# Kernel optimization log

Hardware: AMD Instinct MI355X
Metric: run time of the kernel (lower is better)

## Reference

```python
import jax, jax.numpy as jnp
import numpy as np
import math

B, T, C = 32, 256, 1024
LAYER_ID, NUM_LAYERS = 12, 24
NEG_INF = -1e38


def setup_inputs() -> dict:
    key = jax.random.key(0)
    ks = jax.random.split(key, 5)
    x = jax.random.normal(ks[0], (B, T, C), dtype=jnp.float32)
    # deterministic parameter init, faithful to the torch __init__
    r01 = LAYER_ID / (NUM_LAYERS - 1)          # ratio_0_to_1
    r10 = 1.0 - LAYER_ID / NUM_LAYERS          # ratio_1_to_almost0
    h = jnp.arange(C, dtype=jnp.float32)
    time_decay = -5.0 + 8.0 * (h / (C - 1)) ** (0.7 + 1.3 * r01)
    tf = (jnp.arange(C) + 1) % 3 - 1
    time_first = jnp.full((C,), math.log(0.3), jnp.float32) + 0.5 * tf.astype(jnp.float32)
    xr = (jnp.arange(C, dtype=jnp.float32) / C)[None, None, :]   # [1,1,C]
    time_mix_k = xr ** r10
    time_mix_v = xr ** r10 + 0.3 * r01
    time_mix_r = xr ** (0.5 * r10)
    s = 1.0 / math.sqrt(C)
    Wk = jax.random.normal(ks[1], (C, C), jnp.float32) * s
    Wv = jax.random.normal(ks[2], (C, C), jnp.float32) * s
    Wr = jax.random.normal(ks[3], (C, C), jnp.float32) * s
    Wo = jax.random.normal(ks[4], (C, C), jnp.float32) * s
    return {"x": x, "time_decay": time_decay, "time_first": time_first,
            "time_mix_k": time_mix_k, "time_mix_v": time_mix_v, "time_mix_r": time_mix_r,
            "Wk": Wk, "Wv": Wv, "Wr": Wr, "Wo": Wo}


def wkv(time_decay, time_first, k, v):
    """Numerically-stabilized WKV scan. k,v: [B,T,C]; decay/first: [C]."""
    w = -jnp.exp(time_decay)   # per-channel log-decay (negative)
    u = time_first
    kT = jnp.swapaxes(k, 0, 1)  # [T,B,C]
    vT = jnp.swapaxes(v, 0, 1)

    def step(carry, kv):
        p, q, o = carry                       # p,q: running num/den; o: log scale
        kt, vt = kv                           # [B,C]
        no = jnp.maximum(o, u + kt)
        A = jnp.exp(o - no)
        Bc = jnp.exp(u + kt - no)
        y = (A * p + Bc * vt) / (A * q + Bc)
        no2 = jnp.maximum(w + o, kt)
        A2 = jnp.exp(w + o - no2)
        B2 = jnp.exp(kt - no2)
        return (A2 * p + B2 * vt, A2 * q + B2, no2), y

    init = (jnp.zeros((k.shape[0], k.shape[2]), k.dtype),
            jnp.zeros((k.shape[0], k.shape[2]), k.dtype),
            jnp.full((k.shape[0], k.shape[2]), NEG_INF, k.dtype))
    _, yT = jax.lax.scan(step, init, (kT, vT))
    return jnp.swapaxes(yT, 0, 1)  # [B,T,C]


def reference(x, time_decay, time_first, time_mix_k, time_mix_v, time_mix_r, Wk, Wv, Wr, Wo):
    # time_shift: xx[t] = x[t-1], xx[0] = 0
    xx = jnp.pad(x, ((0, 0), (1, 0), (0, 0)))[:, :-1, :]
    xk = x * time_mix_k + xx * (1.0 - time_mix_k)
    xv = x * time_mix_v + xx * (1.0 - time_mix_v)
    xr = x * time_mix_r + xx * (1.0 - time_mix_r)
    k = jnp.einsum('btc,dc->btd', xk, Wk)
    v = jnp.einsum('btc,dc->btd', xv, Wv)
    r = jnp.einsum('btc,dc->btd', xr, Wr)
    sr = jax.nn.sigmoid(r)
    rwkv = sr * wkv(time_decay, time_first, k, v)
    return jnp.einsum('btc,dc->btd', rwkv, Wo)
```

## Files before the change

kernel.cpp:

```cpp
#include <hip/hip_runtime.h>

#define Bdim 32
#define Tdim 256
#define Cdim 1024

typedef unsigned short u16;
typedef unsigned int u32;
typedef __bf16 bf16x8 __attribute__((ext_vector_type(8)));
typedef float f32x4 __attribute__((ext_vector_type(4)));

__device__ __forceinline__ float bf2f(u32 u) {
    union { u32 i; float f; } v; v.i = u << 16; return v.f;
}
__device__ __forceinline__ u16 f2bf(float f) {
    union { float f; u32 i; } v; v.f = f;
    u32 u = v.i;
    return (u16)((u + 0x7fffu + ((u >> 16) & 1u)) >> 16);
}

__device__ __forceinline__ void gload16(const u16* g, u16* l) {
    __builtin_amdgcn_global_load_lds(
        (__attribute__((address_space(1))) const void*)g,
        (__attribute__((address_space(3))) void*)l, 16, 0, 0);
}

__global__ __launch_bounds__(256) void prep_fused(
    const float* __restrict__ x, const float* __restrict__ tmk,
    const float* __restrict__ tmv, const float* __restrict__ tmr,
    u16* __restrict__ xk, u16* __restrict__ xv, u16* __restrict__ xr,
    const float* __restrict__ w0, const float* __restrict__ w1,
    const float* __restrict__ w2, const float* __restrict__ w3,
    u16* __restrict__ o0, u16* __restrict__ o1,
    u16* __restrict__ o2, u16* __restrict__ o3)
{
    int bid = blockIdx.x;
    if (bid < 4096) {
        int tid = bid * 256 + threadIdx.x;
        int e = tid << 3;
        int c = e & (Cdim - 1);
        int t = (e >> 10) & (Tdim - 1);
        float xf[8], xxf[8], mk[8], mv[8], mr[8];
        *(float4*)(xf)     = *(const float4*)(x + e);
        *(float4*)(xf + 4) = *(const float4*)(x + e + 4);
        if (t != 0) {
            *(float4*)(xxf)     = *(const float4*)(x + e - Cdim);
            *(float4*)(xxf + 4) = *(const float4*)(x + e - Cdim + 4);
        } else {
#pragma unroll
            for (int j = 0; j < 8; j++) xxf[j] = 0.f;
        }
        *(float4*)(mk)     = *(const float4*)(tmk + c);
        *(float4*)(mk + 4) = *(const float4*)(tmk + c + 4);
        *(float4*)(mv)     = *(const float4*)(tmv + c);
        *(float4*)(mv + 4) = *(const float4*)(tmv + c + 4);
        *(float4*)(mr)     = *(const float4*)(tmr + c);
        *(float4*)(mr + 4) = *(const float4*)(tmr + c + 4);
        u16 ok[8], ov[8], orr[8];
#pragma unroll
        for (int j = 0; j < 8; j++) {
            float d = xf[j] - xxf[j];
            ok[j]  = f2bf(xxf[j] + d * mk[j]);
            ov[j]  = f2bf(xxf[j] + d * mv[j]);
            orr[j] = f2bf(xxf[j] + d * mr[j]);
        }
        *(uint4*)(xk + e) = *(const uint4*)ok;
        *(uint4*)(xv + e) = *(const uint4*)ov;
        *(uint4*)(xr + e) = *(const uint4*)orr;
    } else {
        int wb = bid - 4096;
        int m = wb >> 9;
        const float* src; u16* dst;
        switch (m) {
            case 0: src = w0; dst = o0; break;
            case 1: src = w1; dst = o1; break;
            case 2: src = w2; dst = o2; break;
            default: src = w3; dst = o3; break;
        }
        int i = (((wb & 511) << 8) + threadIdx.x) << 3;
        float a[8];
        *(float4*)(a)     = *(const float4*)(src + i);
        *(float4*)(a + 4) = *(const float4*)(src + i + 4);
        u16 o[8];
#pragma unroll
        for (int j = 0; j < 8; j++) o[j] = f2bf(a[j]);
        *(uint4*)(dst + i) = *(const uint4*)o;
    }
}

template <int BF16OUT>
__device__ __forceinline__ void gemm_body(
    const u16* __restrict__ A, const u16* __restrict__ Bw, void* __restrict__ Cout,
    u16* __restrict__ Ls, int bm, int bn)
{
    const int K = Cdim, N = Cdim;
    const int NT = K / 64;
    const int tid = threadIdx.x;
    const int lane = tid & 63, wave = tid >> 6;
    const int wm = (wave & 1) << 6, wn = (wave >> 1) << 6;
    const int fr = lane & 15, quad = lane >> 4;

    const int srow = tid >> 2;
    const int skc = ((((tid & 3) + ((tid >> 3) & 3)) & 3) << 3);
    const u16* ga = A + (size_t)(bm * 128 + srow) * K + skc;
    const u16* gb = Bw + (size_t)(bn * 128 + srow) * K + skc;
    const size_t gstep = (size_t)64 * K;
    const int lw = wave << 9;

    auto stage = [&](int t, int buf) {
        const u16* gat = ga + t * 64;
        const u16* gbt = gb + t * 64;
        u16* base = Ls + buf * 16384 + lw;
        gload16(gat,              base);
        gload16(gat + gstep,      base + 2048);
        gload16(gbt,              base + 4096);
        gload16(gbt + gstep,      base + 4096 + 2048);
        gload16(gat + 32,         base + 8192);
        gload16(gat + 32 + gstep, base + 8192 + 2048);
        gload16(gbt + 32,         base + 12288);
        gload16(gbt + 32 + gstep, base + 12288 + 2048);
    };

    f32x4 acc[4][4];
#pragma unroll
    for (int i = 0; i < 4; i++)
#pragma unroll
        for (int j = 0; j < 4; j++)
            acc[i][j] = (f32x4){0.f, 0.f, 0.f, 0.f};

    const int rq = (((quad - ((fr >> 1) & 3)) & 3) << 3);

    stage(0, 0);
    asm volatile("s_waitcnt vmcnt(0)" ::: "memory");
    __builtin_amdgcn_s_barrier();

#pragma unroll 1
    for (int t = 0; t < NT; ++t) {
        const int buf = t & 1;
        if (t + 1 < NT) stage(t + 1, buf ^ 1);
        const u16* __restrict__ Tb = Ls + buf * 16384;
#pragma unroll
        for (int h = 0; h < 2; h++) {
            const u16* Ah = Tb + h * 8192;
            const u16* Bh = Tb + 4096 + h * 8192;
            bf16x8 af[4], bfr[4];
#pragma unroll
            for (int i = 0; i < 4; i++) {
                af[i]  = *(const bf16x8*)(Ah + (wm + i * 16 + fr) * 32 + rq);
                bfr[i] = *(const bf16x8*)(Bh + (wn + i * 16 + fr) * 32 + rq);
            }
#pragma unroll
            for (int i = 0; i < 4; i++)
#pragma unroll
                for (int j = 0; j < 4; j++)
                    acc[i][j] = __builtin_amdgcn_mfma_f32_16x16x32_bf16(
                        af[i], bfr[j], acc[i][j], 0, 0, 0);
        }
        asm volatile("s_waitcnt vmcnt(0) lgkmcnt(0)" ::: "memory");
        __builtin_amdgcn_s_barrier();
    }

    const int gr0 = bm * 128 + wm + quad * 4;
    const int gc0 = bn * 128 + wn + fr;
#pragma unroll
    for (int i = 0; i < 4; i++)
#pragma unroll
        for (int j = 0; j < 4; j++)
#pragma unroll
            for (int r = 0; r < 4; r++) {
                int gr = gr0 + i * 16 + r;
                int gc = gc0 + j * 16;
                float val = acc[i][j][r];
                if (BF16OUT)
                    ((u16*)Cout)[(size_t)gr * N + gc] = f2bf(val);
                else
                    ((float*)Cout)[(size_t)gr * N + gc] = val;
            }
}

__global__ __launch_bounds__(256) void gemm3_kernel(
    const u16* __restrict__ xk, const u16* __restrict__ xv, const u16* __restrict__ xr,
    const u16* __restrict__ wk, const u16* __restrict__ wv, const u16* __restrict__ wr,
    u16* __restrict__ ck, u16* __restrict__ cv, u16* __restrict__ cr)
{
    __shared__ __align__(16) u16 Ls[2 * 16384];
    const u16* A; const u16* Bw; u16* Cout;
    switch (blockIdx.z) {
        case 0:  A = xk; Bw = wk; Cout = ck; break;
        case 1:  A = xv; Bw = wv; Cout = cv; break;
        default: A = xr; Bw = wr; Cout = cr; break;
    }
    int bx = blockIdx.x;
    gemm_body<1>(A, Bw, (void*)Cout, Ls, bx & 63, bx >> 6);
}

__global__ __launch_bounds__(256) void gemmo_kernel(
    const u16* __restrict__ A, const u16* __restrict__ Bw, float* __restrict__ Cout)
{
    __shared__ __align__(16) u16 Ls[2 * 16384];
    int bx = blockIdx.x;
    gemm_body<0>(A, Bw, (void*)Cout, Ls, bx & 63, bx >> 6);
}

#define WTC 16

#define LOADCHUNK(KA, VA, RA, T0)                                        \
    _Pragma("unroll")                                                    \
    for (int s = 0; s < WTC; s++) {                                      \
        size_t idx = base + (size_t)((T0) + s) * Cdim;                   \
        KA[s] = kb[idx]; VA[s] = vb[idx]; RA[s] = rb[idx];               \
    }

#define COMPCHUNK(KA, VA, RA, T0)                                        \
    _Pragma("unroll")                                                    \
    for (int s = 0; s < WTC; s++) {                                      \
        float kt = bf2f(KA[s]);                                          \
        float vt = bf2f(VA[s]);                                          \
        float rt = bf2f(RA[s]);                                          \
        float uk = u + kt;                                               \
        float no = fmaxf(o, uk);                                         \
        float Ae = __expf(o - no);                                       \
        float Bc = __expf(uk - no);                                      \
        float num = Ae * p + Bc * vt;                                    \
        float den = Ae * q + Bc;                                         \
        float y = num * __builtin_amdgcn_rcpf(den);                      \
        float sr = __builtin_amdgcn_rcpf(1.f + __expf(-rt));             \
        rwkv[base + (size_t)((T0) + s) * Cdim] = f2bf(y * sr);           \
        float wo = w + o;                                                \
        float no2 = fmaxf(wo, kt);                                       \
        float A2 = __expf(wo - no2);                                     \
        float B2 = __expf(kt - no2);                                     \
        p = A2 * p + B2 * vt;                                            \
        q = A2 * q + B2;                                                 \
        o = no2;                                                         \
    }

__global__ __launch_bounds__(64) void wkv_kernel(
    const u16* __restrict__ kb, const u16* __restrict__ vb,
    const u16* __restrict__ rb, const float* __restrict__ td,
    const float* __restrict__ tfirst, u16* __restrict__ rwkv)
{
    int lane = threadIdx.x;
    int blk = blockIdx.x;
    int b = blk >> 4;
    int c = ((blk & 15) << 6) + lane;
    float w = -__expf(td[c]);
    float u = tfirst[c];
    const size_t base = (size_t)b * Tdim * Cdim + c;

    u32 kA[WTC], vA[WTC], rA[WTC];
    u32 kB[WTC], vB[WTC], rB[WTC];
    float p = 0.f, q = 0.f, o = -1e38f;

    LOADCHUNK(kA, vA, rA, 0)
    for (int t0 = 0; t0 < Tdim; t0 += 2 * WTC) {
        LOADCHUNK(kB, vB, rB, t0 + WTC)
        COMPCHUNK(kA, vA, rA, t0)
        if (t0 + 2 * WTC < Tdim) {
            LOADCHUNK(kA, vA, rA, t0 + 2 * WTC)
        }
        COMPCHUNK(kB, vB, rB, t0 + WTC)
    }
}

extern "C" void kernel_launch(void* const* d_in, const int* in_sizes, int n_in,
                              void* d_out, int out_size, void* d_ws, size_t ws_size,
                              hipStream_t stream) {
    (void)in_sizes; (void)n_in; (void)out_size; (void)ws_size;
    const float* x   = (const float*)d_in[0];
    const float* td  = (const float*)d_in[1];
    const float* tfi = (const float*)d_in[2];
    const float* tmk = (const float*)d_in[3];
    const float* tmv = (const float*)d_in[4];
    const float* tmr = (const float*)d_in[5];
    const float* Wk  = (const float*)d_in[6];
    const float* Wv  = (const float*)d_in[7];
    const float* Wr  = (const float*)d_in[8];
    const float* Wo  = (const float*)d_in[9];

    char* ws = (char*)d_ws;
    const size_t MiB = (size_t)1 << 20;
    u16* xk    = (u16*)(ws);
    u16* xv    = (u16*)(ws + 16 * MiB);
    u16* xr    = (u16*)(ws + 32 * MiB);
    u16* wkb   = (u16*)(ws + 48 * MiB);
    u16* wvb   = (u16*)(ws + 50 * MiB);
    u16* wrb   = (u16*)(ws + 52 * MiB);
    u16* wob   = (u16*)(ws + 54 * MiB);
    u16* kb    = (u16*)(ws + 56 * MiB);
    u16* vb    = (u16*)(ws + 72 * MiB);
    u16* rb    = (u16*)(ws + 88 * MiB);
    u16* rwkvb = (u16*)(ws);

    prep_fused<<<6144, 256, 0, stream>>>(x, tmk, tmv, tmr, xk, xv, xr,
                                         Wk, Wv, Wr, Wo, wkb, wvb, wrb, wob);

    gemm3_kernel<<<dim3(512, 1, 3), 256, 0, stream>>>(xk, xv, xr, wkb, wvb, wrb,
                                                      kb, vb, rb);

    wkv_kernel<<<512, 64, 0, stream>>>(kb, vb, rb, td, tfi, rwkvb);

    gemmo_kernel<<<512, 256, 0, stream>>>(rwkvb, wob, (float*)d_out);
}
```

Baseline: 226.9 us.

## Process two channels per thread in WKV scan and use syncthreads in GEMM loop

The WKV kernel now handles two adjacent channels per lane, loading and storing packed 32-bit pairs of bf16 values. This halves the grid to 256 blocks and gives each thread two independent recurrences to interleave, which is meant to hide exp/rcp latency and widen memory accesses. The trade-off is fewer wavefronts on a machine with many CUs, so latency hiding relies on ILP instead of occupancy. Separately, the GEMM's explicit waitcnt+s_barrier pairs are replaced with __syncthreads plus a sched_barrier, which may change how the compiler schedules waits around the LDS pipeline.

```diff
diff --git a/kernel.cpp b/kernel.cpp
--- a/kernel.cpp
+++ b/kernel.cpp
@@ -130,8 +130,8 @@
     const int rq = (((quad - ((fr >> 1) & 3)) & 3) << 3);
 
     stage(0, 0);
-    asm volatile("s_waitcnt vmcnt(0)" ::: "memory");
-    __builtin_amdgcn_s_barrier();
+    __syncthreads();
+    __builtin_amdgcn_sched_barrier(0);
 
 #pragma unroll 1
     for (int t = 0; t < NT; ++t) {
@@ -155,8 +155,8 @@
                     acc[i][j] = __builtin_amdgcn_mfma_f32_16x16x32_bf16(
                         af[i], bfr[j], acc[i][j], 0, 0, 0);
         }
-        asm volatile("s_waitcnt vmcnt(0) lgkmcnt(0)" ::: "memory");
-        __builtin_amdgcn_s_barrier();
+        __syncthreads();
+        __builtin_amdgcn_sched_barrier(0);
     }
 
     const int gr0 = bm * 128 + wm + quad * 4;
@@ -203,35 +203,39 @@
 
 #define WTC 16
 
-#define LOADCHUNK(KA, VA, RA, T0)                                        \
+#define LOADCHUNK2(KA, VA, RA, T0)                                       \
     _Pragma("unroll")                                                    \
     for (int s = 0; s < WTC; s++) {                                      \
-        size_t idx = base + (size_t)((T0) + s) * Cdim;                   \
-        KA[s] = kb[idx]; VA[s] = vb[idx]; RA[s] = rb[idx];               \
-    }
-
-#define COMPCHUNK(KA, VA, RA, T0)                                        \
+        size_t idx = base32 + (size_t)((T0) + s) * cs;                   \
+        KA[s] = k32[idx]; VA[s] = v32[idx]; RA[s] = r32[idx];            \
+    }
+
+#define COMPCHUNK2(KA, VA, RA, T0)                                       \
     _Pragma("unroll")                                                    \
     for (int s = 0; s < WTC; s++) {                                      \
-        float kt = bf2f(KA[s]);                                          \
-        float vt = bf2f(VA[s]);                                          \
-        float rt = bf2f(RA[s]);                                          \
-        float uk = u + kt;                                               \
-        float no = fmaxf(o, uk);                                         \
-        float Ae = __expf(o - no);                                       \
-        float Bc = __expf(uk - no);                                      \
-        float num = Ae * p + Bc * vt;                                    \
-        float den = Ae * q + Bc;                                         \
-        float y = num * __builtin_amdgcn_rcpf(den);                      \
-        float sr = __builtin_amdgcn_rcpf(1.f + __expf(-rt));             \
-        rwkv[base + (size_t)((T0) + s) * Cdim] = f2bf(y * sr);           \
-        float wo = w + o;                                                \
-        float no2 = fmaxf(wo, kt);                                       \
-        float A2 = __expf(wo - no2);                                     \
-        float B2 = __expf(kt - no2);                                     \
-        p = A2 * p + B2 * vt;                                            \
-        q = A2 * q + B2;                                                 \
-        o = no2;                                                         \
+        u32 kk = KA[s], vv = VA[s], rr = RA[s];                          \
+        float kt0 = bf2f(kk), kt1 = bf2f(kk >> 16);                      \
+        float vt0 = bf2f(vv), vt1 = bf2f(vv >> 16);                      \
+        float rt0 = bf2f(rr), rt1 = bf2f(rr >> 16);                      \
+        float uk0 = u0 + kt0,            uk1 = u1 + kt1;                 \
+        float no0 = fmaxf(o0, uk0),      no1 = fmaxf(o1, uk1);           \
+        float Ae0 = __expf(o0 - no0),    Ae1 = __expf(o1 - no1);         \
+        float Bc0 = __expf(uk0 - no0),   Bc1 = __expf(uk1 - no1);        \
+        float nm0 = Ae0 * p0 + Bc0 * vt0, nm1 = Ae1 * p1 + Bc1 * vt1;    \
+        float dn0 = Ae0 * q0 + Bc0,      dn1 = Ae1 * q1 + Bc1;           \
+        float y0 = nm0 * __builtin_amdgcn_rcpf(dn0);                     \
+        float y1 = nm1 * __builtin_amdgcn_rcpf(dn1);                     \
+        float sr0 = __builtin_amdgcn_rcpf(1.f + __expf(-rt0));           \
+        float sr1 = __builtin_amdgcn_rcpf(1.f + __expf(-rt1));           \
+        u32 pk = (u32)f2bf(y0 * sr0) | ((u32)f2bf(y1 * sr1) << 16);      \
+        ow32[base32 + (size_t)((T0) + s) * cs] = pk;                     \
+        float wo0 = w0 + o0,             wo1 = w1 + o1;                  \
+        float n20 = fmaxf(wo0, kt0),     n21 = fmaxf(wo1, kt1);         \
+        float A20 = __expf(wo0 - n20),   A21 = __expf(wo1 - n21);        \
+        float B20 = __expf(kt0 - n20),   B21 = __expf(kt1 - n21);        \
+        p0 = A20 * p0 + B20 * vt0;       p1 = A21 * p1 + B21 * vt1;      \
+        q0 = A20 * q0 + B20;             q1 = A21 * q1 + B21;            \
+        o0 = n20;                        o1 = n21;                       \
     }
 
 __global__ __launch_bounds__(64) void wkv_kernel(
@@ -241,24 +245,30 @@
 {
     int lane = threadIdx.x;
     int blk = blockIdx.x;
-    int b = blk >> 4;
-    int c = ((blk & 15) << 6) + lane;
-    float w = -__expf(td[c]);
-    float u = tfirst[c];
-    const size_t base = (size_t)b * Tdim * Cdim + c;
+    int b = blk >> 3;
+    int c = ((blk & 7) << 7) + (lane << 1);
+    float w0 = -__expf(td[c]),     w1 = -__expf(td[c + 1]);
+    float u0 = tfirst[c],          u1 = tfirst[c + 1];
+    const u32* k32 = (const u32*)kb;
+    const u32* v32 = (const u32*)vb;
+    const u32* r32 = (const u32*)rb;
+    u32* ow32 = (u32*)rwkv;
+    const size_t base32 = ((size_t)b * Tdim * Cdim + c) >> 1;
+    const int cs = Cdim >> 1;
 
     u32 kA[WTC], vA[WTC], rA[WTC];
     u32 kB[WTC], vB[WTC], rB[WTC];
-    float p = 0.f, q = 0.f, o = -1e38f;
-
-    LOADCHUNK(kA, vA, rA, 0)
+    float p0 = 0.f, q0 = 0.f, o0 = -1e38f;
+    float p1 = 0.f, q1 = 0.f, o1 = -1e38f;
+
+    LOADCHUNK2(kA, vA, rA, 0)
     for (int t0 = 0; t0 < Tdim; t0 += 2 * WTC) {
-        LOADCHUNK(kB, vB, rB, t0 + WTC)
-        COMPCHUNK(kA, vA, rA, t0)
+        LOADCHUNK2(kB, vB, rB, t0 + WTC)
+        COMPCHUNK2(kA, vA, rA, t0)
         if (t0 + 2 * WTC < Tdim) {
-            LOADCHUNK(kA, vA, rA, t0 + 2 * WTC)
-        }
-        COMPCHUNK(kB, vB, rB, t0 + WTC)
+            LOADCHUNK2(kA, vA, rA, t0 + 2 * WTC)
+        }
+        COMPCHUNK2(kB, vB, rB, t0 + WTC)
     }
 }
 
@@ -297,7 +307,7 @@
     gemm3_kernel<<<dim3(512, 1, 3), 256, 0, stream>>>(xk, xv, xr, wkb, wvb, wrb,
                                                       kb, vb, rb);
 
-    wkv_kernel<<<512, 64, 0, stream>>>(kb, vb, rb, td, tfi, rwkvb);
+    wkv_kernel<<<256, 64, 0, stream>>>(kb, vb, rb, td, tfi, rwkvb);
 
     gemmo_kernel<<<512, 256, 0, stream>>>(rwkvb, wob, (float*)d_out);
 }
```

Result: slower. 241.2 us (+6.3%).

## Fuse all stages into one cooperative persistent kernel with grid syncs

Applied to the files above, without the earlier changes.

Replaces the four separate launches (prep, 3 GEMMs, WKV scan, output GEMM) with a single cooperative kernel that loops over work items and uses grid.sync between stages. The goal is to remove launch gaps and kernel boundaries. In exchange the grid is capped at 256 or 512 blocks, so each block runs the three GEMMs serially, and the WKV stage uses only 64 of 256 threads per block. Restrict qualifiers and the hand-written waitcnt barriers are replaced with __syncthreads plus sched_barrier, which may change code generation. The old multi-kernel path is kept as a fallback if the cooperative launch fails.

```diff
diff --git a/kernel.cpp b/kernel.cpp
--- a/kernel.cpp
+++ b/kernel.cpp
@@ -1,4 +1,7 @@
 #include <hip/hip_runtime.h>
+#include <hip/hip_cooperative_groups.h>
+
+namespace cg = cooperative_groups;
 
 #define Bdim 32
 #define Tdim 256
@@ -24,18 +27,15 @@
         (__attribute__((address_space(3))) void*)l, 16, 0, 0);
 }
 
-__global__ __launch_bounds__(256) void prep_fused(
-    const float* __restrict__ x, const float* __restrict__ tmk,
-    const float* __restrict__ tmv, const float* __restrict__ tmr,
-    u16* __restrict__ xk, u16* __restrict__ xv, u16* __restrict__ xr,
-    const float* __restrict__ w0, const float* __restrict__ w1,
-    const float* __restrict__ w2, const float* __restrict__ w3,
-    u16* __restrict__ o0, u16* __restrict__ o1,
-    u16* __restrict__ o2, u16* __restrict__ o3)
-{
-    int bid = blockIdx.x;
+__device__ __forceinline__ void prep_body(
+    int bid, int tx,
+    const float* x, const float* tmk, const float* tmv, const float* tmr,
+    u16* xk, u16* xv, u16* xr,
+    const float* w0, const float* w1, const float* w2, const float* w3,
+    u16* o0, u16* o1, u16* o2, u16* o3)
+{
     if (bid < 4096) {
-        int tid = bid * 256 + threadIdx.x;
+        int tid = bid * 256 + tx;
         int e = tid << 3;
         int c = e & (Cdim - 1);
         int t = (e >> 10) & (Tdim - 1);
@@ -76,7 +76,7 @@
             case 2: src = w2; dst = o2; break;
             default: src = w3; dst = o3; break;
         }
-        int i = (((wb & 511) << 8) + threadIdx.x) << 3;
+        int i = (((wb & 511) << 8) + tx) << 3;
         float a[8];
         *(float4*)(a)     = *(const float4*)(src + i);
         *(float4*)(a + 4) = *(const float4*)(src + i + 4);
@@ -89,8 +89,7 @@
 
 template <int BF16OUT>
 __device__ __forceinline__ void gemm_body(
-    const u16* __restrict__ A, const u16* __restrict__ Bw, void* __restrict__ Cout,
-    u16* __restrict__ Ls, int bm, int bn)
+    const u16* A, const u16* Bw, void* Cout, u16* Ls, int bm, int bn)
 {
     const int K = Cdim, N = Cdim;
     const int NT = K / 64;
@@ -130,14 +129,14 @@
     const int rq = (((quad - ((fr >> 1) & 3)) & 3) << 3);
 
     stage(0, 0);
-    asm volatile("s_waitcnt vmcnt(0)" ::: "memory");
-    __builtin_amdgcn_s_barrier();
+    __syncthreads();
+    __builtin_amdgcn_sched_barrier(0);
 
 #pragma unroll 1
     for (int t = 0; t < NT; ++t) {
         const int buf = t & 1;
         if (t + 1 < NT) stage(t + 1, buf ^ 1);
-        const u16* __restrict__ Tb = Ls + buf * 16384;
+        const u16* Tb = Ls + buf * 16384;
 #pragma unroll
         for (int h = 0; h < 2; h++) {
             const u16* Ah = Tb + h * 8192;
@@ -155,8 +154,8 @@
                     acc[i][j] = __builtin_amdgcn_mfma_f32_16x16x32_bf16(
                         af[i], bfr[j], acc[i][j], 0, 0, 0);
         }
-        asm volatile("s_waitcnt vmcnt(0) lgkmcnt(0)" ::: "memory");
-        __builtin_amdgcn_s_barrier();
+        __syncthreads();
+        __builtin_amdgcn_sched_barrier(0);
     }
 
     const int gr0 = bm * 128 + wm + quad * 4;
@@ -177,37 +176,13 @@
             }
 }
 
-__global__ __launch_bounds__(256) void gemm3_kernel(
-    const u16* __restrict__ xk, const u16* __restrict__ xv, const u16* __restrict__ xr,
-    const u16* __restrict__ wk, const u16* __restrict__ wv, const u16* __restrict__ wr,
-    u16* __restrict__ ck, u16* __restrict__ cv, u16* __restrict__ cr)
-{
-    __shared__ __align__(16) u16 Ls[2 * 16384];
-    const u16* A; const u16* Bw; u16* Cout;
-    switch (blockIdx.z) {
-        case 0:  A = xk; Bw = wk; Cout = ck; break;
-        case 1:  A = xv; Bw = wv; Cout = cv; break;
-        default: A = xr; Bw = wr; Cout = cr; break;
-    }
-    int bx = blockIdx.x;
-    gemm_body<1>(A, Bw, (void*)Cout, Ls, bx & 63, bx >> 6);
-}
-
-__global__ __launch_bounds__(256) void gemmo_kernel(
-    const u16* __restrict__ A, const u16* __restrict__ Bw, float* __restrict__ Cout)
-{
-    __shared__ __align__(16) u16 Ls[2 * 16384];
-    int bx = blockIdx.x;
-    gemm_body<0>(A, Bw, (void*)Cout, Ls, bx & 63, bx >> 6);
-}
-
 #define WTC 16
 
 #define LOADCHUNK(KA, VA, RA, T0)                                        \
     _Pragma("unroll")                                                    \
     for (int s = 0; s < WTC; s++) {                                      \
         size_t idx = base + (size_t)((T0) + s) * Cdim;                   \
-        KA[s] = kb[idx]; VA[s] = vb[idx]; RA[s] = rb[idx];               \
+        KA[s] = kbf[idx]; VA[s] = vbf[idx]; RA[s] = rbf[idx];            \
     }
 
 #define COMPCHUNK(KA, VA, RA, T0)                                        \
@@ -234,13 +209,11 @@
         o = no2;                                                         \
     }
 
-__global__ __launch_bounds__(64) void wkv_kernel(
-    const u16* __restrict__ kb, const u16* __restrict__ vb,
-    const u16* __restrict__ rb, const float* __restrict__ td,
-    const float* __restrict__ tfirst, u16* __restrict__ rwkv)
-{
-    int lane = threadIdx.x;
-    int blk = blockIdx.x;
+__device__ __forceinline__ void wkv_body(
+    int blk, int lane,
+    const u16* kbf, const u16* vbf, const u16* rbf,
+    const float* td, const float* tfirst, u16* rwkv)
+{
     int b = blk >> 4;
     int c = ((blk & 15) << 6) + lane;
     float w = -__expf(td[c]);
@@ -260,6 +233,92 @@
         }
         COMPCHUNK(kB, vB, rB, t0 + WTC)
     }
+}
+
+__global__ __launch_bounds__(256, 2) void fused_all(
+    const float* x, const float* td, const float* tfi,
+    const float* tmk, const float* tmv, const float* tmr,
+    const float* Wk, const float* Wv, const float* Wr, const float* Wo,
+    u16* xk, u16* xv, u16* xr,
+    u16* wkb, u16* wvb, u16* wrb, u16* wob,
+    u16* kbuf, u16* vbuf, u16* rbuf,
+    u16* rwkvb, float* outp)
+{
+    __shared__ __align__(16) u16 Ls[2 * 16384];
+    cg::grid_group grid = cg::this_grid();
+    const int bx = blockIdx.x;
+    const int tx = threadIdx.x;
+    const int nb = gridDim.x;
+
+    for (int v = bx; v < 6144; v += nb)
+        prep_body(v, tx, x, tmk, tmv, tmr, xk, xv, xr,
+                  Wk, Wv, Wr, Wo, wkb, wvb, wrb, wob);
+    __threadfence();
+    grid.sync();
+    __threadfence();
+
+    for (int v = bx; v < 512; v += nb) {
+        const int bm = v & 63, bn = v >> 6;
+        gemm_body<1>(xk, wkb, (void*)kbuf, Ls, bm, bn);
+        gemm_body<1>(xv, wvb, (void*)vbuf, Ls, bm, bn);
+        gemm_body<1>(xr, wrb, (void*)rbuf, Ls, bm, bn);
+    }
+    __threadfence();
+    grid.sync();
+    __threadfence();
+
+    for (int v = bx; v < 512; v += nb)
+        if (tx < 64)
+            wkv_body(v, tx, kbuf, vbuf, rbuf, td, tfi, rwkvb);
+    __threadfence();
+    grid.sync();
+    __threadfence();
+
+    for (int v = bx; v < 512; v += nb) {
+        const int bm = v & 63, bn = v >> 6;
+        gemm_body<0>(rwkvb, wob, (void*)outp, Ls, bm, bn);
+    }
+}
+
+__global__ __launch_bounds__(256) void prep_fused(
+    const float* x, const float* tmk, const float* tmv, const float* tmr,
+    u16* xk, u16* xv, u16* xr,
+    const float* w0, const float* w1, const float* w2, const float* w3,
+    u16* o0, u16* o1, u16* o2, u16* o3)
+{
+    prep_body(blockIdx.x, threadIdx.x, x, tmk, tmv, tmr, xk, xv, xr,
+              w0, w1, w2, w3, o0, o1, o2, o3);
+}
+
+__global__ __launch_bounds__(256) void gemm3_kernel(
+    const u16* xk, const u16* xv, const u16* xr,
+    const u16* wk, const u16* wv, const u16* wr,
+    u16* ck, u16* cv, u16* cr)
+{
+    __shared__ __align__(16) u16 Ls[2 * 16384];
+    const u16* A; const u16* Bw; u16* Cout;
+    switch (blockIdx.z) {
+        case 0:  A = xk; Bw = wk; Cout = ck; break;
+        case 1:  A = xv; Bw = wv; Cout = cv; break;
+        default: A = xr; Bw = wr; Cout = cr; break;
+    }
+    int bx = blockIdx.x;
+    gemm_body<1>(A, Bw, (void*)Cout, Ls, bx & 63, bx >> 6);
+}
+
+__global__ __launch_bounds__(64) void wkv_kernel(
+    const u16* kb, const u16* vb, const u16* rb,
+    const float* td, const float* tfirst, u16* rwkv)
+{
+    wkv_body(blockIdx.x, threadIdx.x, kb, vb, rb, td, tfirst, rwkv);
+}
+
+__global__ __launch_bounds__(256) void gemmo_kernel(
+    const u16* A, const u16* Bw, float* Cout)
+{
+    __shared__ __align__(16) u16 Ls[2 * 16384];
+    int bx = blockIdx.x;
+    gemm_body<0>(A, Bw, (void*)Cout, Ls, bx & 63, bx >> 6);
 }
 
 extern "C" void kernel_launch(void* const* d_in, const int* in_sizes, int n_in,
@@ -286,18 +345,39 @@
     u16* wvb   = (u16*)(ws + 50 * MiB);
     u16* wrb   = (u16*)(ws + 52 * MiB);
     u16* wob   = (u16*)(ws + 54 * MiB);
-    u16* kb    = (u16*)(ws + 56 * MiB);
-    u16* vb    = (u16*)(ws + 72 * MiB);
-    u16* rb    = (u16*)(ws + 88 * MiB);
+    u16* kbuf  = (u16*)(ws + 56 * MiB);
+    u16* vbuf  = (u16*)(ws + 72 * MiB);
+    u16* rbuf  = (u16*)(ws + 88 * MiB);
     u16* rwkvb = (u16*)(ws);
-
-    prep_fused<<<6144, 256, 0, stream>>>(x, tmk, tmv, tmr, xk, xv, xr,
-                                         Wk, Wv, Wr, Wo, wkb, wvb, wrb, wob);
-
-    gemm3_kernel<<<dim3(512, 1, 3), 256, 0, stream>>>(xk, xv, xr, wkb, wvb, wrb,
-                                                      kb, vb, rb);
-
-    wkv_kernel<<<512, 64, 0, stream>>>(kb, vb, rb, td, tfi, rwkvb);
-
-    gemmo_kernel<<<512, 256, 0, stream>>>(rwkvb, wob, (float*)d_out);
-}
+    float* outp = (float*)d_out;
+
+    static int coopGrid = 0;
+    if (coopGrid == 0) {
+        int nbpc = 0;
+        if (hipOccupancyMaxActiveBlocksPerMultiprocessor(&nbpc, fused_all, 256, 0)
+                != hipSuccess || nbpc < 1)
+            nbpc = 1;
+        coopGrid = (nbpc >= 2) ? 512 : 256;
+    }
+
+    void* ka[] = {
+        (void*)&x, (void*)&td, (void*)&tfi, (void*)&tmk, (void*)&tmv,
+        (void*)&tmr, (void*)&Wk, (void*)&Wv, (void*)&Wr, (void*)&Wo,
+        (void*)&xk, (void*)&xv, (void*)&xr, (void*)&wkb, (void*)&wvb,
+        (void*)&wrb, (void*)&wob, (void*)&kbuf, (void*)&vbuf, (void*)&rbuf,
+        (void*)&rwkvb, (void*)&outp
+    };
+    hipError_t cerr = hipLaunchCooperativeKernel((void*)fused_all,
+                                                 dim3(coopGrid), dim3(256),
+                                                 ka, 0, stream);
+    if (cerr != hipSuccess) {
+        (void)hipGetLastError();
+        prep_fused<<<6144, 256, 0, stream>>>(x, tmk, tmv, tmr, xk, xv, xr,
+                                             Wk, Wv, Wr, Wo, wkb, wvb, wrb, wob);
+        gemm3_kernel<<<dim3(512, 1, 3), 256, 0, stream>>>(xk, xv, xr,
+                                                          wkb, wvb, wrb,
+                                                          kbuf, vbuf, rbuf);
+        wkv_kernel<<<512, 64, 0, stream>>>(kbuf, vbuf, rbuf, td, tfi, rwkvb);
+        gemmo_kernel<<<512, 256, 0, stream>>>(rwkvb, wob, outp);
+    }
+}
```

Result: slower. 530.6 us (+133.8%).
